# Kernel tuning notes

Measured on AMD Instinct MI355X. Metric: run time of the kernel, lower is better.

Reference implementation:

```python
import jax, jax.numpy as jnp
import numpy as np

B, S, D = 8, 1024, 768
H = 12
DH = D // H  # 64
SCALE = 1.0 / (D ** 0.5)  # module scales by full embedding_dim, not head_dim


def setup_inputs() -> dict:
    key = jax.random.key(0)
    ks = jax.random.split(key, 7)
    std = 1.0 / np.sqrt(D)
    return {
        "x": jax.random.normal(ks[0], (B, S, D), dtype=jnp.float32),
        "Wq": jax.random.uniform(ks[1], (D, D), jnp.float32, -std, std),
        "bq": jax.random.uniform(ks[2], (D,), jnp.float32, -std, std),
        "Wk": jax.random.uniform(ks[3], (D, D), jnp.float32, -std, std),
        "bk": jax.random.uniform(ks[4], (D,), jnp.float32, -std, std),
        "Wv": jax.random.uniform(ks[5], (D, D), jnp.float32, -std, std),
        "bv": jax.random.uniform(ks[6], (D,), jnp.float32, -std, std),
    }


def reference(x, Wq, bq, Wk, bk, Wv, bv):
    b, s, d = x.shape
    # projections; torch.chunk(dim=-1) == reshape last dim to [H, DH]
    q = (x @ Wq + bq).reshape(b, s, H, DH)
    k = (x @ Wk + bk).reshape(b, s, H, DH)
    v = (x @ Wv + bv).reshape(b, s, H, DH)
    # per-head scores [b, h, s, s], scaled by sqrt(embedding_dim) per source
    scores = jnp.einsum("bqhd,bkhd->bhqk", q, k) * SCALE
    attn = jax.nn.softmax(scores, axis=-1)
    out = jnp.einsum("bhqk,bkhd->bqhd", attn, v)
    # concat heads back along last dim (order matches chunk order)
    return out.reshape(b, s, d)
```

## Files before the change

kernel.cpp:

```cpp
#include <hip/hip_runtime.h>
#include <cstdint>
#include <cstddef>

typedef unsigned short u16;
typedef unsigned int u32;
typedef unsigned char u8;

using bfx8 = __attribute__((ext_vector_type(8))) __bf16;
using floatx16 = __attribute__((ext_vector_type(16))) float;

static constexpr int kS = 1024;
static constexpr int kD = 768;
static constexpr int kH = 12;
static constexpr int kDH = 64;
#define SCALE 0.036084391824351614f

__device__ __forceinline__ u16 f2bf(float f) {
    u32 u = __float_as_uint(f);
    return (u16)((u + 0x7fffu + ((u >> 16) & 1u)) >> 16);
}

__device__ __forceinline__ void gld16(const void* g, void* l) {
    __builtin_amdgcn_global_load_lds(
        (__attribute__((address_space(1))) const u32*)g,
        (__attribute__((address_space(3))) u32*)l, 16, 0, 0);
}

__global__ __launch_bounds__(256) void cvt_x(const float* __restrict__ x, u16* __restrict__ xb) {
    int i = (blockIdx.x * 256 + threadIdx.x) * 4;
    float4 v = *(const float4*)(x + i);
    u32 lo = (u32)f2bf(v.x) | ((u32)f2bf(v.y) << 16);
    u32 hi = (u32)f2bf(v.z) | ((u32)f2bf(v.w) << 16);
    *(uint2*)(xb + i) = make_uint2(lo, hi);
}

__global__ __launch_bounds__(256) void cvt_w(const float* __restrict__ w0, const float* __restrict__ w1,
                                             const float* __restrict__ w2, u16* __restrict__ wt) {
    __shared__ float t[32][33];
    const float* W = blockIdx.z == 0 ? w0 : (blockIdx.z == 1 ? w1 : w2);
    u16* dst = wt + (size_t)blockIdx.z * kD * kD;
    int k0 = blockIdx.x * 32, n0 = blockIdx.y * 32;
    int tx = threadIdx.x, ty = threadIdx.y;
#pragma unroll
    for (int j = 0; j < 4; j++)
        t[ty + j * 8][tx] = W[(size_t)(k0 + ty + j * 8) * kD + n0 + tx];
    __syncthreads();
#pragma unroll
    for (int j = 0; j < 4; j++)
        dst[(size_t)(n0 + ty + j * 8) * kD + k0 + tx] = f2bf(t[tx][ty + j * 8]);
}

__global__ __launch_bounds__(256) void proj(const u16* __restrict__ xb, const u16* __restrict__ wt,
                                            const float* __restrict__ bq, const float* __restrict__ bk,
                                            const float* __restrict__ bvp,
                                            u16* __restrict__ qb, u16* __restrict__ kb, u16* __restrict__ vt) {
    __shared__ u16 As[128 * 64];
    __shared__ u16 Bs[128 * 64];
    int m0 = blockIdx.x * 128;
    int n0g = blockIdx.y * 128;
    int t = threadIdx.x;
    int w = t >> 6, lane = t & 63;
    int l31 = lane & 31, hi = lane >> 5;
    int wm = (w & 1) * 64, wn = (w >> 1) * 64;
    int rloc8 = lane >> 3, p8 = lane & 7;
    const u16* Brow = wt + (size_t)n0g * kD;
    int swz = (l31 & 7) ^ ((l31 >> 4) << 2);
    floatx16 acc[2][2] = {};
    for (int ks = 0; ks < kD; ks += 64) {
        __syncthreads();
#pragma unroll
        for (int i = 0; i < 4; i++) {
            int j = w * 4 + i;
            int r = 8 * j + rloc8;
            int chw = p8 ^ rloc8 ^ (((j >> 1) & 1) << 2);
            gld16(xb + (size_t)(m0 + r) * kD + ks + chw * 8, &As[j * 512]);
            gld16(Brow + (size_t)r * kD + ks + chw * 8, &Bs[j * 512]);
        }
        __syncthreads();
#pragma unroll
        for (int s = 0; s < 4; s++) {
            int tc = ((s * 2 + hi) ^ swz) * 8;
            bfx8 a[2], bf[2];
#pragma unroll
            for (int i = 0; i < 2; i++) {
                a[i] = *(const bfx8*)&As[(wm + i * 32 + l31) * 64 + tc];
                bf[i] = *(const bfx8*)&Bs[(wn + i * 32 + l31) * 64 + tc];
            }
#pragma unroll
            for (int i = 0; i < 2; i++)
#pragma unroll
                for (int j = 0; j < 2; j++)
                    acc[i][j] = __builtin_amdgcn_mfma_f32_32x32x16_bf16(a[i], bf[j], acc[i][j], 0, 0, 0);
        }
    }
    int zz = blockIdx.y / 6;
    int nl0 = (blockIdx.y - zz * 6) * 128;
    const float* bias = zz == 0 ? bq : (zz == 1 ? bk : bvp);
    float mul = zz == 0 ? SCALE : 1.0f;
#pragma unroll
    for (int j = 0; j < 2; j++) {
        int nl = nl0 + wn + j * 32 + l31;
        float bb = bias[nl];
#pragma unroll
        for (int i = 0; i < 2; i++) {
            int mbase = m0 + wm + i * 32 + 4 * hi;
            if (zz < 2) {
                u16* dst = zz == 0 ? qb : kb;
#pragma unroll
                for (int reg = 0; reg < 16; reg++) {
                    int m = mbase + (reg & 3) + 8 * (reg >> 2);
                    dst[(size_t)m * kD + nl] = f2bf((acc[i][j][reg] + bb) * mul);
                }
            } else {
                int hh = nl >> 6, dh = nl & 63;
#pragma unroll
                for (int g = 0; g < 4; g++) {
                    int m = mbase + 8 * g;
                    int bi = m >> 10, s = m & 1023;
                    u32 lo = (u32)f2bf(acc[i][j][4 * g + 0] + bb) | ((u32)f2bf(acc[i][j][4 * g + 1] + bb) << 16);
                    u32 h2 = (u32)f2bf(acc[i][j][4 * g + 2] + bb) | ((u32)f2bf(acc[i][j][4 * g + 3] + bb) << 16);
                    *(uint2*)&vt[(((size_t)bi * kH + hh) * kDH + dh) * kS + s] = make_uint2(lo, h2);
                }
            }
        }
    }
}

__global__ __launch_bounds__(256, 4) void attn(const u16* __restrict__ qb, const u16* __restrict__ kb,
                                               const u16* __restrict__ vt, float* __restrict__ out) {
    __shared__ u16 KPs[128 * 64];
    __shared__ u16 Vs[64 * 128];
    __shared__ float Lw[2][64];
    int q0 = blockIdx.x * 64;
    int bh = blockIdx.y;
    int b = bh / kH, h = bh % kH;
    int t = threadIdx.x, w = t >> 6, lane = t & 63;
    int l31 = lane & 31, hi = lane >> 5;
    int qh = w & 1, kh = w >> 1;

    bfx8 qf[4];
    {
        const u16* qrow = qb + (size_t)(b * kS + q0 + qh * 32 + l31) * kD + h * kDH + hi * 8;
#pragma unroll
        for (int f = 0; f < 4; f++) qf[f] = *(const bfx8*)(qrow + f * 16);
    }

    int qrl = qh * 32 + l31;
    int pswz = (l31 & 15) ^ ((l31 >> 4) << 3);
    int kswz = (l31 & 7) ^ ((l31 >> 4) << 2);
    int vswz = (l31 & 15) ^ ((l31 >> 4) << 3);
    float rsum = 0.f;
    floatx16 oacc = {};

    for (int kt = 0; kt < 8; kt++) {
        int kk0 = kt * 128;
        __syncthreads();
#pragma unroll
        for (int i = 0; i < 4; i++) {
            int jj = 4 * w + i;
            int r = 8 * jj + (lane >> 3);
            int c = (lane & 7) ^ (lane >> 3) ^ (((jj >> 1) & 1) << 2);
            gld16(kb + (size_t)(b * kS + kk0 + r) * kD + h * kDH + c * 8, &KPs[jj * 512]);
        }
#pragma unroll
        for (int i = 0; i < 4; i++) {
            int jj = 4 * w + i;
            int r = 4 * jj + (lane >> 4);
            int c = (lane & 15) ^ (r & 15) ^ (((jj >> 2) & 1) << 3);
            gld16(vt + (((size_t)b * kH + h) * kDH + r) * kS + kk0 + c * 8, &Vs[jj * 512]);
        }
        __syncthreads();

        floatx16 sacc[2] = {};
#pragma unroll
        for (int s = 0; s < 4; s++) {
#pragma unroll
            for (int fm = 0; fm < 2; fm++) {
                int row = kh * 64 + fm * 32 + l31;
                int tc = ((s * 2 + hi) ^ kswz) * 8;
                bfx8 ak = *(const bfx8*)&KPs[row * 64 + tc];
                sacc[fm] = __builtin_amdgcn_mfma_f32_32x32x16_bf16(ak, qf[s], sacc[fm], 0, 0, 0);
            }
        }
        __syncthreads();

        u8* prow = (u8*)KPs + qrl * 256;
#pragma unroll
        for (int fm = 0; fm < 2; fm++) {
#pragma unroll
            for (int g = 0; g < 4; g++) {
                float p0 = __expf(sacc[fm][4 * g + 0]);
                float p1 = __expf(sacc[fm][4 * g + 1]);
                float p2 = __expf(sacc[fm][4 * g + 2]);
                float p3 = __expf(sacc[fm][4 * g + 3]);
                rsum += (p0 + p1) + (p2 + p3);
                u32 lo = (u32)f2bf(p0) | ((u32)f2bf(p1) << 16);
                u32 h2 = (u32)f2bf(p2) | ((u32)f2bf(p3) << 16);
                int c16 = kh * 8 + fm * 4 + g;
                *(uint2*)(prow + ((c16 ^ pswz) * 2 + hi) * 8) = make_uint2(lo, h2);
            }
        }
        __syncthreads();

#pragma unroll
        for (int s = 0; s < 8; s++) {
            bfx8 ap = *(const bfx8*)(prow + ((s * 2 + hi) ^ pswz) * 16);
            bfx8 bv = *(const bfx8*)((const u8*)Vs + (kh * 32 + l31) * 256 + (((s * 2 + hi) ^ vswz) * 16));
            oacc = __builtin_amdgcn_mfma_f32_32x32x16_bf16(ap, bv, oacc, 0, 0, 0);
        }
    }

    rsum += __shfl_xor(rsum, 32, 64);
    if (lane < 32) Lw[kh][qh * 32 + lane] = rsum;
    __syncthreads();
#pragma unroll
    for (int g = 0; g < 4; g++) {
#pragma unroll
        for (int r2 = 0; r2 < 4; r2++) {
            int qloc = qh * 32 + r2 + 8 * g + 4 * hi;
            float linv = 1.0f / (Lw[0][qloc] + Lw[1][qloc]);
            out[(size_t)(b * kS + q0 + qloc) * kD + h * kDH + kh * 32 + l31] = oacc[4 * g + r2] * linv;
        }
    }
}

extern "C" void kernel_launch(void* const* d_in, const int* in_sizes, int n_in,
                              void* d_out, int out_size, void* d_ws, size_t ws_size,
                              hipStream_t stream) {
    const float* x  = (const float*)d_in[0];
    const float* Wq = (const float*)d_in[1];
    const float* bq = (const float*)d_in[2];
    const float* Wk = (const float*)d_in[3];
    const float* bk = (const float*)d_in[4];
    const float* Wv = (const float*)d_in[5];
    const float* bv = (const float*)d_in[6];
    float* out = (float*)d_out;

    u16* ws = (u16*)d_ws;
    u16* xb = ws;
    u16* wt = xb + 6291456;
    u16* qb = wt + 1769472;
    u16* kb = qb + 6291456;
    u16* vt = kb + 6291456;

    cvt_x<<<dim3(6144), dim3(256), 0, stream>>>(x, xb);
    cvt_w<<<dim3(24, 24, 3), dim3(32, 8), 0, stream>>>(Wq, Wk, Wv, wt);
    proj<<<dim3(64, 18), dim3(256), 0, stream>>>(xb, wt, bq, bk, bv, qb, kb, vt);
    attn<<<dim3(16, 96), dim3(256), 0, stream>>>(qb, kb, vt, out);
}
```

Baseline: 187.2 us.

## Fuse all stages into one persistent cooperative kernel with grid syncs

Replaces the four separate launches (x conversion, weight transpose/convert, QKV projection, attention) with a single persistent cooperative kernel. Blocks loop over job indices for each stage and share one LDS union, with grid.sync between stages. This removes per-launch overhead and inter-kernel gaps. In exchange it adds grid-wide barriers and forces the projection and attention stages to run at the occupancy of the combined kernel, with a grid capped at 1024 blocks, which can cause tail imbalance (for example 1152 projection jobs).

```diff
diff --git a/kernel.cpp b/kernel.cpp
--- a/kernel.cpp
+++ b/kernel.cpp
@@ -1,6 +1,9 @@
 #include <hip/hip_runtime.h>
+#include <hip/hip_cooperative_groups.h>
 #include <cstdint>
 #include <cstddef>
+
+namespace cg = cooperative_groups;
 
 typedef unsigned short u16;
 typedef unsigned int u32;
@@ -26,39 +29,47 @@
         (__attribute__((address_space(3))) u32*)l, 16, 0, 0);
 }
 
-__global__ __launch_bounds__(256) void cvt_x(const float* __restrict__ x, u16* __restrict__ xb) {
-    int i = (blockIdx.x * 256 + threadIdx.x) * 4;
+union SharedU {
+    struct { u16 As[128 * 64]; u16 Bs[128 * 64]; } p;
+    struct { u16 KPs[128 * 64]; u16 Vs[64 * 128]; float Lw[2][64]; } a;
+    struct { float t[32][33]; } w;
+};
+
+
+__device__ void do_cvt_x(int job, int t, const float* __restrict__ x, u16* __restrict__ xb) {
+    int i = (job * 256 + t) * 4;
     float4 v = *(const float4*)(x + i);
     u32 lo = (u32)f2bf(v.x) | ((u32)f2bf(v.y) << 16);
     u32 hi = (u32)f2bf(v.z) | ((u32)f2bf(v.w) << 16);
     *(uint2*)(xb + i) = make_uint2(lo, hi);
 }
 
-__global__ __launch_bounds__(256) void cvt_w(const float* __restrict__ w0, const float* __restrict__ w1,
-                                             const float* __restrict__ w2, u16* __restrict__ wt) {
-    __shared__ float t[32][33];
-    const float* W = blockIdx.z == 0 ? w0 : (blockIdx.z == 1 ? w1 : w2);
-    u16* dst = wt + (size_t)blockIdx.z * kD * kD;
-    int k0 = blockIdx.x * 32, n0 = blockIdx.y * 32;
-    int tx = threadIdx.x, ty = threadIdx.y;
+__device__ void do_cvt_w(SharedU* sh, int job, int t, const float* __restrict__ w0,
+                         const float* __restrict__ w1, const float* __restrict__ w2,
+                         u16* __restrict__ wt) {
+    int z = job / 576, r = job % 576;
+    int kx = r % 24, ny = r / 24;
+    const float* W = z == 0 ? w0 : (z == 1 ? w1 : w2);
+    u16* dst = wt + (size_t)z * kD * kD;
+    int k0 = kx * 32, n0 = ny * 32;
+    int tx = t & 31, ty = t >> 5;
+    __syncthreads();
 #pragma unroll
     for (int j = 0; j < 4; j++)
-        t[ty + j * 8][tx] = W[(size_t)(k0 + ty + j * 8) * kD + n0 + tx];
+        sh->w.t[ty + j * 8][tx] = W[(size_t)(k0 + ty + j * 8) * kD + n0 + tx];
     __syncthreads();
 #pragma unroll
     for (int j = 0; j < 4; j++)
-        dst[(size_t)(n0 + ty + j * 8) * kD + k0 + tx] = f2bf(t[tx][ty + j * 8]);
-}
-
-__global__ __launch_bounds__(256) void proj(const u16* __restrict__ xb, const u16* __restrict__ wt,
-                                            const float* __restrict__ bq, const float* __restrict__ bk,
-                                            const float* __restrict__ bvp,
-                                            u16* __restrict__ qb, u16* __restrict__ kb, u16* __restrict__ vt) {
-    __shared__ u16 As[128 * 64];
-    __shared__ u16 Bs[128 * 64];
-    int m0 = blockIdx.x * 128;
-    int n0g = blockIdx.y * 128;
-    int t = threadIdx.x;
+        dst[(size_t)(n0 + ty + j * 8) * kD + k0 + tx] = f2bf(sh->w.t[tx][ty + j * 8]);
+}
+
+__device__ void do_proj(SharedU* sh, int job, int t, const u16* __restrict__ xb,
+                        const u16* __restrict__ wt, const float* __restrict__ bq,
+                        const float* __restrict__ bk, const float* __restrict__ bvp,
+                        u16* __restrict__ qb, u16* __restrict__ kb, u16* __restrict__ vt) {
+    int m0 = (job & 63) * 128;
+    int by = job >> 6;
+    int n0g = by * 128;
     int w = t >> 6, lane = t & 63;
     int l31 = lane & 31, hi = lane >> 5;
     int wm = (w & 1) * 64, wn = (w >> 1) * 64;
@@ -73,8 +84,8 @@
             int j = w * 4 + i;
             int r = 8 * j + rloc8;
             int chw = p8 ^ rloc8 ^ (((j >> 1) & 1) << 2);
-            gld16(xb + (size_t)(m0 + r) * kD + ks + chw * 8, &As[j * 512]);
-            gld16(Brow + (size_t)r * kD + ks + chw * 8, &Bs[j * 512]);
+            gld16(xb + (size_t)(m0 + r) * kD + ks + chw * 8, &sh->p.As[j * 512]);
+            gld16(Brow + (size_t)r * kD + ks + chw * 8, &sh->p.Bs[j * 512]);
         }
         __syncthreads();
 #pragma unroll
@@ -83,8 +94,8 @@
             bfx8 a[2], bf[2];
 #pragma unroll
             for (int i = 0; i < 2; i++) {
-                a[i] = *(const bfx8*)&As[(wm + i * 32 + l31) * 64 + tc];
-                bf[i] = *(const bfx8*)&Bs[(wn + i * 32 + l31) * 64 + tc];
+                a[i] = *(const bfx8*)&sh->p.As[(wm + i * 32 + l31) * 64 + tc];
+                bf[i] = *(const bfx8*)&sh->p.Bs[(wn + i * 32 + l31) * 64 + tc];
             }
 #pragma unroll
             for (int i = 0; i < 2; i++)
@@ -93,8 +104,8 @@
                     acc[i][j] = __builtin_amdgcn_mfma_f32_32x32x16_bf16(a[i], bf[j], acc[i][j], 0, 0, 0);
         }
     }
-    int zz = blockIdx.y / 6;
-    int nl0 = (blockIdx.y - zz * 6) * 128;
+    int zz = by / 6;
+    int nl0 = (by - zz * 6) * 128;
     const float* bias = zz == 0 ? bq : (zz == 1 ? bk : bvp);
     float mul = zz == 0 ? SCALE : 1.0f;
 #pragma unroll
@@ -126,15 +137,13 @@
     }
 }
 
-__global__ __launch_bounds__(256, 4) void attn(const u16* __restrict__ qb, const u16* __restrict__ kb,
-                                               const u16* __restrict__ vt, float* __restrict__ out) {
-    __shared__ u16 KPs[128 * 64];
-    __shared__ u16 Vs[64 * 128];
-    __shared__ float Lw[2][64];
-    int q0 = blockIdx.x * 64;
-    int bh = blockIdx.y;
+__device__ void do_attn(SharedU* sh, int job, int t, const u16* __restrict__ qb,
+                        const u16* __restrict__ kb, const u16* __restrict__ vt,
+                        float* __restrict__ out) {
+    int q0 = (job & 15) * 64;
+    int bh = job >> 4;
     int b = bh / kH, h = bh % kH;
-    int t = threadIdx.x, w = t >> 6, lane = t & 63;
+    int w = t >> 6, lane = t & 63;
     int l31 = lane & 31, hi = lane >> 5;
     int qh = w & 1, kh = w >> 1;
 
@@ -160,14 +169,14 @@
             int jj = 4 * w + i;
             int r = 8 * jj + (lane >> 3);
             int c = (lane & 7) ^ (lane >> 3) ^ (((jj >> 1) & 1) << 2);
-            gld16(kb + (size_t)(b * kS + kk0 + r) * kD + h * kDH + c * 8, &KPs[jj * 512]);
+            gld16(kb + (size_t)(b * kS + kk0 + r) * kD + h * kDH + c * 8, &sh->a.KPs[jj * 512]);
         }
 #pragma unroll
         for (int i = 0; i < 4; i++) {
             int jj = 4 * w + i;
             int r = 4 * jj + (lane >> 4);
             int c = (lane & 15) ^ (r & 15) ^ (((jj >> 2) & 1) << 3);
-            gld16(vt + (((size_t)b * kH + h) * kDH + r) * kS + kk0 + c * 8, &Vs[jj * 512]);
+            gld16(vt + (((size_t)b * kH + h) * kDH + r) * kS + kk0 + c * 8, &sh->a.Vs[jj * 512]);
         }
         __syncthreads();
 
@@ -178,13 +187,13 @@
             for (int fm = 0; fm < 2; fm++) {
                 int row = kh * 64 + fm * 32 + l31;
                 int tc = ((s * 2 + hi) ^ kswz) * 8;
-                bfx8 ak = *(const bfx8*)&KPs[row * 64 + tc];
+                bfx8 ak = *(const bfx8*)&sh->a.KPs[row * 64 + tc];
                 sacc[fm] = __builtin_amdgcn_mfma_f32_32x32x16_bf16(ak, qf[s], sacc[fm], 0, 0, 0);
             }
         }
         __syncthreads();
 
-        u8* prow = (u8*)KPs + qrl * 256;
+        u8* prow = (u8*)sh->a.KPs + qrl * 256;
 #pragma unroll
         for (int fm = 0; fm < 2; fm++) {
 #pragma unroll
@@ -205,23 +214,48 @@
 #pragma unroll
         for (int s = 0; s < 8; s++) {
             bfx8 ap = *(const bfx8*)(prow + ((s * 2 + hi) ^ pswz) * 16);
-            bfx8 bv = *(const bfx8*)((const u8*)Vs + (kh * 32 + l31) * 256 + (((s * 2 + hi) ^ vswz) * 16));
+            bfx8 bv = *(const bfx8*)((const u8*)sh->a.Vs + (kh * 32 + l31) * 256 + (((s * 2 + hi) ^ vswz) * 16));
             oacc = __builtin_amdgcn_mfma_f32_32x32x16_bf16(ap, bv, oacc, 0, 0, 0);
         }
     }
 
     rsum += __shfl_xor(rsum, 32, 64);
-    if (lane < 32) Lw[kh][qh * 32 + lane] = rsum;
+    if (lane < 32) sh->a.Lw[kh][qh * 32 + lane] = rsum;
     __syncthreads();
 #pragma unroll
     for (int g = 0; g < 4; g++) {
 #pragma unroll
         for (int r2 = 0; r2 < 4; r2++) {
             int qloc = qh * 32 + r2 + 8 * g + 4 * hi;
-            float linv = 1.0f / (Lw[0][qloc] + Lw[1][qloc]);
+            float linv = 1.0f / (sh->a.Lw[0][qloc] + sh->a.Lw[1][qloc]);
             out[(size_t)(b * kS + q0 + qloc) * kD + h * kDH + kh * 32 + l31] = oacc[4 * g + r2] * linv;
         }
     }
+}
+
+__global__ __launch_bounds__(256, 4) void fused(
+        const float* __restrict__ x, const float* __restrict__ Wq, const float* __restrict__ bq,
+        const float* __restrict__ Wk, const float* __restrict__ bk, const float* __restrict__ Wv,
+        const float* __restrict__ bv, float* __restrict__ out,
+        u16* __restrict__ xb, u16* __restrict__ wt, u16* __restrict__ qb,
+        u16* __restrict__ kb, u16* __restrict__ vt) {
+    __shared__ SharedU sh;
+    cg::grid_group grid = cg::this_grid();
+    int t = threadIdx.x;
+    int g = gridDim.x;
+
+    for (int job = blockIdx.x; job < 6144; job += g) do_cvt_x(job, t, x, xb);
+    for (int job = blockIdx.x; job < 1728; job += g) do_cvt_w(&sh, job, t, Wq, Wk, Wv, wt);
+
+    grid.sync();
+
+    for (int job = blockIdx.x; job < 1152; job += g)
+        do_proj(&sh, job, t, xb, wt, bq, bk, bv, qb, kb, vt);
+
+    grid.sync();
+
+    for (int job = blockIdx.x; job < 1536; job += g)
+        do_attn(&sh, job, t, qb, kb, vt, out);
 }
 
 extern "C" void kernel_launch(void* const* d_in, const int* in_sizes, int n_in,
@@ -243,8 +277,15 @@
     u16* kb = qb + 6291456;
     u16* vt = kb + 6291456;
 
-    cvt_x<<<dim3(6144), dim3(256), 0, stream>>>(x, xb);
-    cvt_w<<<dim3(24, 24, 3), dim3(32, 8), 0, stream>>>(Wq, Wk, Wv, wt);
-    proj<<<dim3(64, 18), dim3(256), 0, stream>>>(xb, wt, bq, bk, bv, qb, kb, vt);
-    attn<<<dim3(16, 96), dim3(256), 0, stream>>>(qb, kb, vt, out);
-}
+    int nb = 0;
+    if (hipOccupancyMaxActiveBlocksPerMultiprocessor(&nb, (const void*)fused, 256, 0) != hipSuccess || nb <= 0)
+        nb = 3;
+    if (nb > 4) nb = 4;
+    int grid = nb * 256;
+    if (grid > 1024) grid = 1024;
+
+    void* args[] = {(void*)&x, (void*)&Wq, (void*)&bq, (void*)&Wk, (void*)&bk,
+                    (void*)&Wv, (void*)&bv, (void*)&out, (void*)&xb, (void*)&wt,
+                    (void*)&qb, (void*)&kb, (void*)&vt};
+    hipLaunchCooperativeKernel((const void*)fused, dim3(grid), dim3(256), args, 0, stream);
+}
```

After: 426.2 us. +127.7%, slower.
